# Kernel optimization log

Hardware: AMD Instinct MI355X
Metric: run time of the kernel (lower is better)

## Reference

```python
import jax, jax.numpy as jnp
import numpy as np

NUM_STEPS = 8
THRESHOLD = 0.5


def _glorot(key, shape):
    fan_in = shape[0]
    return jax.random.normal(key, shape, dtype=jnp.float32) / np.sqrt(fan_in).astype(np.float32)


def setup_inputs() -> dict:
    key = jax.random.key(0)
    ks = jax.random.split(key, 24)
    B, APM = 2048, 32           # molecules, atoms per molecule
    N = B * APM                 # 65536 nodes
    E = N * 4                   # 262144 directed edges
    NF, EF, NH, EH, MA = 64, 16, 128, 128, 256
    inp = {}
    inp['mol_a_reprs'] = jax.random.normal(ks[0], (B, MA), dtype=jnp.float32)
    inp['node_features'] = jax.random.normal(ks[1], (N, NF), dtype=jnp.float32)
    inp['edge_features'] = jax.random.normal(ks[2], (E, EF), dtype=jnp.float32)
    inp['node_hidden0'] = jnp.zeros((N, NH), dtype=jnp.float32)
    inp['edge_hidden0'] = jnp.zeros((E, EH), dtype=jnp.float32)
    inp['edges'] = jax.random.randint(ks[3], (2, E), 0, N, dtype=jnp.int32)
    inp['batch_indices'] = jnp.repeat(jnp.arange(B, dtype=jnp.int32), APM)  # sorted, in-range
    # MPN weights (no bias)
    inp['W1'] = _glorot(ks[4], (NF, EH))   # src node features -> edge hidden
    inp['W2'] = _glorot(ks[5], (EF, EH))   # edge features -> edge hidden
    inp['W3'] = _glorot(ks[6], (NH, EH))   # src node hidden -> edge hidden
    inp['U1'] = _glorot(ks[7], (NF, NH))   # node features -> node hidden
    inp['U2'] = _glorot(ks[8], (EH, NH))   # aggregated edge hidden -> node hidden
    # pick-atom MLP: (MA+NH)->256->128->64->1
    inp['M1w'] = _glorot(ks[9], (MA + NH, 256)); inp['M1b'] = jnp.zeros((256,), jnp.float32)
    inp['M2w'] = _glorot(ks[10], (256, 128));    inp['M2b'] = jnp.zeros((128,), jnp.float32)
    inp['M3w'] = _glorot(ks[11], (128, 64));     inp['M3b'] = jnp.zeros((64,), jnp.float32)
    inp['M4w'] = _glorot(ks[12], (64, 1));       inp['M4b'] = jnp.zeros((1,), jnp.float32)
    return inp


def _mpn(node_features, edge_features, node_h, edge_h, src, dst, W1, W2, W3, U1, U2):
    N = node_features.shape[0]
    W1x_src = node_features[src] @ W1          # [E, EH], loop-invariant
    W2e = edge_features @ W2                   # [E, EH], loop-invariant
    U1x = node_features @ U1                   # [N, NH], loop-invariant
    for _ in range(NUM_STEPS):
        agg = jax.ops.segment_sum(edge_h, dst, num_segments=N)   # [N, EH]
        node_h = jax.nn.relu(U1x + agg @ U2)                     # [N, NH]
        edge_h = jax.nn.relu(W1x_src + W2e + node_h[src] @ W3)   # [E, EH]
    return node_h


def reference(mol_a_reprs, node_features, edge_features, node_hidden0, edge_hidden0,
              edges, batch_indices, W1, W2, W3, U1, U2,
              M1w, M1b, M2w, M2b, M3w, M3b, M4w, M4b):
    src, dst = edges[0], edges[1]
    node_h = _mpn(node_features, edge_features, node_hidden0, edge_hidden0,
                  src, dst, W1, W2, W3, U1, U2)
    b_atom_mol_a = mol_a_reprs[batch_indices]                    # index_select gather [N, MA]
    x = jnp.concatenate([node_h, b_atom_mol_a], axis=1)          # [N, NH+MA]
    x = jax.nn.relu(x @ M1w + M1b)
    x = jax.nn.relu(x @ M2w + M2b)
    x = jax.nn.relu(x @ M3w + M3b)
    p = jax.nn.sigmoid(x @ M4w + M4b)                            # [N, 1]
    return p >= THRESHOLD
```

## Files before the change

kernel.cpp:

```cpp
#include <hip/hip_runtime.h>
#include <cstddef>

#define NF 64
#define EF 16
#define NH 128
#define EH 128
#define MA 256

static inline int ceil_div(int a, int b) { return (a + b - 1) / b; }

__global__ __launch_bounds__(256) void gemm128_kernel(
    const float* __restrict__ A, const float* __restrict__ Bw,
    float* __restrict__ C,
    const float* __restrict__ addR, const int* __restrict__ addIdx,
    const float* __restrict__ bias, const int* __restrict__ gatherA,
    int M, int K, int Nc, int doRelu, int reluA)
{
    __shared__ float As[16][132];
    __shared__ float Bs[16][132];
    const int tid = threadIdx.x;
    const int tx = tid & 15;
    const int ty = tid >> 4;
    const int m0 = blockIdx.y << 7;
    const int n0 = blockIdx.x << 7;

    const int lr = tid >> 1;
    const int lc = (tid & 1) << 3;
    const int br = tid >> 4;
    const int bc = (tid & 15) << 3;

    float acc[8][8];
#pragma unroll
    for (int i = 0; i < 8; ++i)
#pragma unroll
        for (int j = 0; j < 8; ++j) acc[i][j] = 0.0f;

    int arow = gatherA ? gatherA[m0 + lr] : (m0 + lr);
    const float* aptr = A + (size_t)arow * K + lc;

    for (int k0 = 0; k0 < K; k0 += 16) {
        float4 a0 = *(const float4*)(aptr + k0);
        float4 a1 = *(const float4*)(aptr + k0 + 4);
        float4 b0 = *(const float4*)(Bw + (size_t)(k0 + br) * Nc + n0 + bc);
        float4 b1 = *(const float4*)(Bw + (size_t)(k0 + br) * Nc + n0 + bc + 4);
        if (reluA) {
            a0.x = fmaxf(a0.x, 0.f); a0.y = fmaxf(a0.y, 0.f); a0.z = fmaxf(a0.z, 0.f); a0.w = fmaxf(a0.w, 0.f);
            a1.x = fmaxf(a1.x, 0.f); a1.y = fmaxf(a1.y, 0.f); a1.z = fmaxf(a1.z, 0.f); a1.w = fmaxf(a1.w, 0.f);
        }
        __syncthreads();
        As[lc + 0][lr] = a0.x; As[lc + 1][lr] = a0.y; As[lc + 2][lr] = a0.z; As[lc + 3][lr] = a0.w;
        As[lc + 4][lr] = a1.x; As[lc + 5][lr] = a1.y; As[lc + 6][lr] = a1.z; As[lc + 7][lr] = a1.w;
        *(float4*)&Bs[br][bc] = b0;
        *(float4*)&Bs[br][bc + 4] = b1;
        __syncthreads();
#pragma unroll
        for (int kk = 0; kk < 16; ++kk) {
            float4 av0 = *(const float4*)&As[kk][ty * 8];
            float4 av1 = *(const float4*)&As[kk][ty * 8 + 4];
            float4 bv0 = *(const float4*)&Bs[kk][tx * 8];
            float4 bv1 = *(const float4*)&Bs[kk][tx * 8 + 4];
            float a[8] = {av0.x, av0.y, av0.z, av0.w, av1.x, av1.y, av1.z, av1.w};
            float b[8] = {bv0.x, bv0.y, bv0.z, bv0.w, bv1.x, bv1.y, bv1.z, bv1.w};
#pragma unroll
            for (int i = 0; i < 8; ++i)
#pragma unroll
                for (int j = 0; j < 8; ++j)
                    acc[i][j] = fmaf(a[i], b[j], acc[i][j]);
        }
    }

    const int c = n0 + tx * 8;
    float4 bvl = make_float4(0.f, 0.f, 0.f, 0.f), bvh = bvl;
    if (bias) { bvl = *(const float4*)(bias + c); bvh = *(const float4*)(bias + c + 4); }
#pragma unroll
    for (int i = 0; i < 8; ++i) {
        int r = m0 + ty * 8 + i;
        float4 vl = make_float4(acc[i][0], acc[i][1], acc[i][2], acc[i][3]);
        float4 vh = make_float4(acc[i][4], acc[i][5], acc[i][6], acc[i][7]);
        if (addR) {
            int ar = addIdx ? addIdx[r] : r;
            float4 al = *(const float4*)(addR + (size_t)ar * Nc + c);
            float4 ah = *(const float4*)(addR + (size_t)ar * Nc + c + 4);
            vl.x += al.x; vl.y += al.y; vl.z += al.z; vl.w += al.w;
            vh.x += ah.x; vh.y += ah.y; vh.z += ah.z; vh.w += ah.w;
        }
        vl.x += bvl.x; vl.y += bvl.y; vl.z += bvl.z; vl.w += bvl.w;
        vh.x += bvh.x; vh.y += bvh.y; vh.z += bvh.z; vh.w += bvh.w;
        if (doRelu) {
            vl.x = fmaxf(vl.x, 0.f); vl.y = fmaxf(vl.y, 0.f); vl.z = fmaxf(vl.z, 0.f); vl.w = fmaxf(vl.w, 0.f);
            vh.x = fmaxf(vh.x, 0.f); vh.y = fmaxf(vh.y, 0.f); vh.z = fmaxf(vh.z, 0.f); vh.w = fmaxf(vh.w, 0.f);
        }
        *(float4*)(C + (size_t)r * Nc + c) = vl;
        *(float4*)(C + (size_t)r * Nc + c + 4) = vh;
    }
}

__global__ __launch_bounds__(256, 2) void fused_step_kernel(
    const float* __restrict__ nodeT_in, const float* __restrict__ W2eS,
    const int* __restrict__ rp, const int* __restrict__ srcS,
    const float* __restrict__ U1x, const float* __restrict__ U2,
    const float* __restrict__ nodePre, const float* __restrict__ W3,
    float* __restrict__ nodeT_out, float* __restrict__ node_h_out,
    int writeNodeH, int doGemm2)
{
    __shared__ float As[128][132];
    __shared__ float Bs[16][132];
    const int tid = threadIdx.x;
    const int m0 = blockIdx.x << 7;

    {
        const int cx = (tid & 31) << 2;
        const int ry = tid >> 5;
        for (int rg = 0; rg < 16; ++rg) {
            const int row = rg * 8 + ry;
            const int n = m0 + row;
            const int p0 = rp[n], p1 = rp[n + 1];
            float4 s = make_float4(0.f, 0.f, 0.f, 0.f);
            for (int p = p0; p < p1; ++p) {
                const int sn = srcS[p];
                float4 t = *(const float4*)(nodeT_in + (size_t)sn * EH + cx);
                float4 w = *(const float4*)(W2eS + (size_t)p * EH + cx);
                s.x += fmaxf(t.x + w.x, 0.f);
                s.y += fmaxf(t.y + w.y, 0.f);
                s.z += fmaxf(t.z + w.z, 0.f);
                s.w += fmaxf(t.w + w.w, 0.f);
            }
            As[cx + 0][row] = s.x;
            As[cx + 1][row] = s.y;
            As[cx + 2][row] = s.z;
            As[cx + 3][row] = s.w;
        }
    }
    __syncthreads();

    const int tx = tid & 15, ty = tid >> 4;
    const int br = tid >> 4, bc = (tid & 15) << 3;

    float acc[8][8];
#pragma unroll
    for (int i = 0; i < 8; ++i)
#pragma unroll
        for (int j = 0; j < 8; ++j) acc[i][j] = 0.0f;

#define FUSED_GEMM(WPTR)                                                          \
    for (int k0 = 0; k0 < 128; k0 += 16) {                                        \
        float4 b0 = *(const float4*)(WPTR + (size_t)(k0 + br) * 128 + bc);        \
        float4 b1 = *(const float4*)(WPTR + (size_t)(k0 + br) * 128 + bc + 4);    \
        __syncthreads();                                                          \
        *(float4*)&Bs[br][bc] = b0;                                               \
        *(float4*)&Bs[br][bc + 4] = b1;                                           \
        __syncthreads();                                                          \
        _Pragma("unroll")                                                         \
        for (int kk = 0; kk < 16; ++kk) {                                         \
            float4 av0 = *(const float4*)&As[k0 + kk][ty * 8];                    \
            float4 av1 = *(const float4*)&As[k0 + kk][ty * 8 + 4];                \
            float4 bv0 = *(const float4*)&Bs[kk][tx * 8];                         \
            float4 bv1 = *(const float4*)&Bs[kk][tx * 8 + 4];                     \
            float a[8] = {av0.x, av0.y, av0.z, av0.w, av1.x, av1.y, av1.z, av1.w};\
            float b[8] = {bv0.x, bv0.y, bv0.z, bv0.w, bv1.x, bv1.y, bv1.z, bv1.w};\
            _Pragma("unroll")                                                     \
            for (int i = 0; i < 8; ++i)                                           \
                _Pragma("unroll")                                                 \
                for (int j = 0; j < 8; ++j)                                       \
                    acc[i][j] = fmaf(a[i], b[j], acc[i][j]);                      \
        }                                                                         \
    }

    FUSED_GEMM(U2)

    const int c = tx * 8;
#pragma unroll
    for (int i = 0; i < 8; ++i) {
        const int r = m0 + ty * 8 + i;
        float4 u0 = *(const float4*)(U1x + (size_t)r * NH + c);
        float4 u1 = *(const float4*)(U1x + (size_t)r * NH + c + 4);
        acc[i][0] = fmaxf(acc[i][0] + u0.x, 0.f);
        acc[i][1] = fmaxf(acc[i][1] + u0.y, 0.f);
        acc[i][2] = fmaxf(acc[i][2] + u0.z, 0.f);
        acc[i][3] = fmaxf(acc[i][3] + u0.w, 0.f);
        acc[i][4] = fmaxf(acc[i][4] + u1.x, 0.f);
        acc[i][5] = fmaxf(acc[i][5] + u1.y, 0.f);
        acc[i][6] = fmaxf(acc[i][6] + u1.z, 0.f);
        acc[i][7] = fmaxf(acc[i][7] + u1.w, 0.f);
    }
    if (writeNodeH) {
#pragma unroll
        for (int i = 0; i < 8; ++i) {
            const int r = m0 + ty * 8 + i;
            *(float4*)(node_h_out + (size_t)r * NH + c) =
                make_float4(acc[i][0], acc[i][1], acc[i][2], acc[i][3]);
            *(float4*)(node_h_out + (size_t)r * NH + c + 4) =
                make_float4(acc[i][4], acc[i][5], acc[i][6], acc[i][7]);
        }
    }
    if (!doGemm2) return;

    __syncthreads();
#pragma unroll
    for (int i = 0; i < 8; ++i)
#pragma unroll
        for (int j = 0; j < 8; ++j)
            As[tx * 8 + j][ty * 8 + i] = acc[i][j];
    __syncthreads();

#pragma unroll
    for (int i = 0; i < 8; ++i)
#pragma unroll
        for (int j = 0; j < 8; ++j) acc[i][j] = 0.0f;

    FUSED_GEMM(W3)
#undef FUSED_GEMM

#pragma unroll
    for (int i = 0; i < 8; ++i) {
        const int r = m0 + ty * 8 + i;
        float4 p0 = *(const float4*)(nodePre + (size_t)r * EH + c);
        float4 p1 = *(const float4*)(nodePre + (size_t)r * EH + c + 4);
        *(float4*)(nodeT_out + (size_t)r * EH + c) =
            make_float4(acc[i][0] + p0.x, acc[i][1] + p0.y, acc[i][2] + p0.z, acc[i][3] + p0.w);
        *(float4*)(nodeT_out + (size_t)r * EH + c + 4) =
            make_float4(acc[i][4] + p1.x, acc[i][5] + p1.y, acc[i][6] + p1.z, acc[i][7] + p1.w);
    }
}

__global__ __launch_bounds__(256) void hist_kernel(const int* __restrict__ dst, int* __restrict__ deg, int E) {
    int e = blockIdx.x * 256 + threadIdx.x;
    if (e < E) atomicAdd(&deg[dst[e]], 1);
}

__global__ __launch_bounds__(256) void scan_block_kernel(const int* __restrict__ deg, int* __restrict__ rp,
                                                         int* __restrict__ bsum) {
    __shared__ int buf[256];
    int tid = threadIdx.x;
    int i = blockIdx.x * 256 + tid;
    int v = deg[i];
    buf[tid] = v;
    __syncthreads();
    for (int off = 1; off < 256; off <<= 1) {
        int t = (tid >= off) ? buf[tid - off] : 0;
        __syncthreads();
        buf[tid] += t;
        __syncthreads();
    }
    rp[i] = buf[tid] - v;
    if (tid == 255) bsum[blockIdx.x] = buf[255];
}

__global__ __launch_bounds__(256) void scan_top_kernel(const int* __restrict__ bsum, int* __restrict__ boff,
                                                       int* __restrict__ rp, int N) {
    __shared__ int buf[256];
    int tid = threadIdx.x;
    int v = bsum[tid];
    buf[tid] = v;
    __syncthreads();
    for (int off = 1; off < 256; off <<= 1) {
        int t = (tid >= off) ? buf[tid - off] : 0;
        __syncthreads();
        buf[tid] += t;
        __syncthreads();
    }
    boff[tid] = buf[tid] - v;
    if (tid == 255) rp[N] = buf[255];
}

__global__ __launch_bounds__(256) void scan_add_kernel(int* __restrict__ rp, int* __restrict__ cursor,
                                                       const int* __restrict__ boff) {
    int tid = threadIdx.x;
    int i = blockIdx.x * 256 + tid;
    int v = rp[i] + boff[blockIdx.x];
    rp[i] = v;
    cursor[i] = v;
}

__global__ __launch_bounds__(256) void scatter_kernel(const int* __restrict__ dst, const int* __restrict__ src,
                                                      int* __restrict__ cursor,
                                                      int* __restrict__ eid, int* __restrict__ srcS, int E) {
    int e = blockIdx.x * 256 + threadIdx.x;
    if (e < E) {
        int p = atomicAdd(&cursor[dst[e]], 1);
        eid[p] = e;
        srcS[p] = src[e];
    }
}

__global__ __launch_bounds__(256) void x3final_kernel(const float* __restrict__ x2, const float* __restrict__ M3w,
                                                      const float* __restrict__ b3, const float* __restrict__ M4w,
                                                      const float* __restrict__ b4, int* __restrict__ out) {
    __shared__ float As[16][132];
    __shared__ float Bs[16][68];
    __shared__ float red[128][17];
    const int tid = threadIdx.x;
    const int tx = tid & 15;
    const int ty = tid >> 4;
    const int m0 = blockIdx.x << 7;
    const int lr = tid >> 1, lc = (tid & 1) << 3;
    const int br = tid >> 4, bc = (tid & 15) << 2;

    float acc[8][4];
#pragma unroll
    for (int i = 0; i < 8; ++i)
#pragma unroll
        for (int j = 0; j < 4; ++j) acc[i][j] = 0.0f;

    const float* aptr = x2 + (size_t)(m0 + lr) * 128 + lc;
    for (int k0 = 0; k0 < 128; k0 += 16) {
        float4 a0 = *(const float4*)(aptr + k0);
        float4 a1 = *(const float4*)(aptr + k0 + 4);
        float4 bv = *(const float4*)(M3w + (size_t)(k0 + br) * 64 + bc);
        __syncthreads();
        As[lc + 0][lr] = a0.x; As[lc + 1][lr] = a0.y; As[lc + 2][lr] = a0.z; As[lc + 3][lr] = a0.w;
        As[lc + 4][lr] = a1.x; As[lc + 5][lr] = a1.y; As[lc + 6][lr] = a1.z; As[lc + 7][lr] = a1.w;
        *(float4*)&Bs[br][bc] = bv;
        __syncthreads();
#pragma unroll
        for (int kk = 0; kk < 16; ++kk) {
            float4 av0 = *(const float4*)&As[kk][ty * 8];
            float4 av1 = *(const float4*)&As[kk][ty * 8 + 4];
            float4 bv0 = *(const float4*)&Bs[kk][tx * 4];
            float a[8] = {av0.x, av0.y, av0.z, av0.w, av1.x, av1.y, av1.z, av1.w};
            float b[4] = {bv0.x, bv0.y, bv0.z, bv0.w};
#pragma unroll
            for (int i = 0; i < 8; ++i)
#pragma unroll
                for (int j = 0; j < 4; ++j)
                    acc[i][j] = fmaf(a[i], b[j], acc[i][j]);
        }
    }

    const int c = tx * 4;
    float4 b3v = *(const float4*)(b3 + c);
    float4 w4v = *(const float4*)(M4w + c);
#pragma unroll
    for (int i = 0; i < 8; ++i) {
        float p = fmaxf(acc[i][0] + b3v.x, 0.f) * w4v.x
                + fmaxf(acc[i][1] + b3v.y, 0.f) * w4v.y
                + fmaxf(acc[i][2] + b3v.z, 0.f) * w4v.z
                + fmaxf(acc[i][3] + b3v.w, 0.f) * w4v.w;
        red[ty * 8 + i][tx] = p;
    }
    __syncthreads();
    if (tid < 128) {
        float z = b4[0];
#pragma unroll
        for (int j = 0; j < 16; ++j) z += red[tid][j];
        out[m0 + tid] = z >= 0.f ? 1 : 0;
    }
}

extern "C" void kernel_launch(void* const* d_in, const int* in_sizes, int n_in,
                              void* d_out, int out_size, void* d_ws, size_t ws_size,
                              hipStream_t stream)
{
    const float* mol_a = (const float*)d_in[0];
    const float* nf    = (const float*)d_in[1];
    const float* ef    = (const float*)d_in[2];
    const int*   edges = (const int*)d_in[5];
    const int*   batch = (const int*)d_in[6];
    const float* W1  = (const float*)d_in[7];
    const float* W2  = (const float*)d_in[8];
    const float* W3  = (const float*)d_in[9];
    const float* U1  = (const float*)d_in[10];
    const float* U2  = (const float*)d_in[11];
    const float* M1w = (const float*)d_in[12];
    const float* M1b = (const float*)d_in[13];
    const float* M2w = (const float*)d_in[14];
    const float* M2b = (const float*)d_in[15];
    const float* M3w = (const float*)d_in[16];
    const float* M3b = (const float*)d_in[17];
    const float* M4w = (const float*)d_in[18];
    const float* M4b = (const float*)d_in[19];

    const int N = in_sizes[3] / NH;
    const int E = in_sizes[4] / EH;
    const int B = in_sizes[0] / MA;
    const int* srcp = edges;
    const int* dstp = edges + E;

    char* ws = (char*)d_ws;
    size_t off = 0;
    auto alloc = [&](size_t bytes) -> char* {
        char* p = ws + off;
        off = (off + bytes + 255) & ~(size_t)255;
        return p;
    };
    int* deg     = (int*)alloc((size_t)N * 4);
    int* rp      = (int*)alloc(((size_t)N + 1) * 4);
    int* cursor  = (int*)alloc((size_t)N * 4);
    int* bsum    = (int*)alloc(256 * 4);
    int* boff    = (int*)alloc(256 * 4);
    int* eid     = (int*)alloc((size_t)E * 4);
    int* srcS    = (int*)alloc((size_t)E * 4);
    float* nodePre = (float*)alloc((size_t)N * EH * 4);
    float* U1x     = (float*)alloc((size_t)N * NH * 4);
    float* node_h  = (float*)alloc((size_t)N * NH * 4);
    float* nodeTa  = (float*)alloc((size_t)N * EH * 4);
    float* nodeTb  = (float*)alloc((size_t)N * EH * 4);
    float* molPart = (float*)alloc((size_t)B * 256 * 4);
    float* W2eS    = (float*)alloc((size_t)E * EH * 4);
    float* x1 = (float*)W2eS;
    float* x2 = nodeTa;

    hipMemsetAsync(deg, 0, (size_t)N * 4, stream);
    hist_kernel<<<ceil_div(E, 256), 256, 0, stream>>>(dstp, deg, E);
    scan_block_kernel<<<N / 256, 256, 0, stream>>>(deg, rp, bsum);
    scan_top_kernel<<<1, 256, 0, stream>>>(bsum, boff, rp, N);
    scan_add_kernel<<<N / 256, 256, 0, stream>>>(rp, cursor, boff);
    scatter_kernel<<<ceil_div(E, 256), 256, 0, stream>>>(dstp, srcp, cursor, eid, srcS, E);

    gemm128_kernel<<<dim3(1, N / 128), 256, 0, stream>>>(nf, W1, nodePre, nullptr, nullptr, nullptr, nullptr, N, NF, EH, 0, 0);
    gemm128_kernel<<<dim3(1, E / 128), 256, 0, stream>>>(ef, W2, W2eS, nullptr, nullptr, nullptr, eid, E, EF, EH, 0, 0);
    gemm128_kernel<<<dim3(1, N / 128), 256, 0, stream>>>(nf, U1, U1x, nullptr, nullptr, nullptr, nullptr, N, NF, NH, 0, 0);

    gemm128_kernel<<<dim3(1, N / 128), 256, 0, stream>>>(U1x, W3, nodeTa, nodePre, nullptr, nullptr, nullptr, N, NH, EH, 0, 1);

    float* curT = nodeTa;
    float* nxtT = nodeTb;
    for (int s = 0; s < 6; ++s) {
        fused_step_kernel<<<N / 128, 256, 0, stream>>>(curT, W2eS, rp, srcS, U1x, U2, nodePre, W3,
                                                       nxtT, nullptr, 0, 1);
        float* t = curT; curT = nxtT; nxtT = t;
    }
    fused_step_kernel<<<N / 128, 256, 0, stream>>>(curT, W2eS, rp, srcS, U1x, U2, nodePre, W3,
                                                   nxtT, node_h, 1, 0);

    gemm128_kernel<<<dim3(2, B / 128), 256, 0, stream>>>(mol_a, M1w + 128 * 256, molPart, nullptr, nullptr, M1b, nullptr, B, MA, 256, 0, 0);
    gemm128_kernel<<<dim3(2, N / 128), 256, 0, stream>>>(node_h, M1w, x1, molPart, batch, nullptr, nullptr, N, NH, 256, 1, 0);
    gemm128_kernel<<<dim3(1, N / 128), 256, 0, stream>>>(x1, M2w, x2, nullptr, nullptr, M2b, nullptr, N, 256, 128, 1, 0);
    x3final_kernel<<<N / 128, 256, 0, stream>>>(x2, M3w, M3b, M4w, M4b, (int*)d_out);
}
```

Baseline: 1.448 ms.

## Recompute edge-feature projection on the fly and split fused step into agg+GEMMs

Drops the precomputed E×128 W2e buffer. Edge features are permuted once into dst-sorted order (16 floats per edge), and each aggregation pass recomputes ef·W2 with W2 held in registers. This cuts per-step traffic from streaming 128 MB of W2eS to 16 MB plus extra FMAs. The fused per-step kernel is also split into an aggregation kernel and two separate 64-row-tile GEMMs. That adds intermediate round-trips through global memory for agg and node_h but gives smaller tiles and more blocks.

```diff
diff --git a/kernel.cpp b/kernel.cpp
--- a/kernel.cpp
+++ b/kernel.cpp
@@ -9,60 +9,57 @@
 
 static inline int ceil_div(int a, int b) { return (a + b - 1) / b; }
 
-__global__ __launch_bounds__(256) void gemm128_kernel(
+__global__ __launch_bounds__(256) void gemm64_kernel(
     const float* __restrict__ A, const float* __restrict__ Bw,
     float* __restrict__ C,
     const float* __restrict__ addR, const int* __restrict__ addIdx,
-    const float* __restrict__ bias, const int* __restrict__ gatherA,
+    const float* __restrict__ bias,
     int M, int K, int Nc, int doRelu, int reluA)
 {
-    __shared__ float As[16][132];
+    __shared__ float As[16][68];
     __shared__ float Bs[16][132];
     const int tid = threadIdx.x;
     const int tx = tid & 15;
     const int ty = tid >> 4;
-    const int m0 = blockIdx.y << 7;
+    const int m0 = blockIdx.y << 6;
     const int n0 = blockIdx.x << 7;
 
-    const int lr = tid >> 1;
-    const int lc = (tid & 1) << 3;
+    const int lr = tid >> 2;
+    const int lc = (tid & 3) << 2;
     const int br = tid >> 4;
     const int bc = (tid & 15) << 3;
 
-    float acc[8][8];
-#pragma unroll
-    for (int i = 0; i < 8; ++i)
+    float acc[4][8];
+#pragma unroll
+    for (int i = 0; i < 4; ++i)
 #pragma unroll
         for (int j = 0; j < 8; ++j) acc[i][j] = 0.0f;
 
-    int arow = gatherA ? gatherA[m0 + lr] : (m0 + lr);
-    const float* aptr = A + (size_t)arow * K + lc;
+    const float* aptr = A + (size_t)(m0 + lr) * K + lc;
 
     for (int k0 = 0; k0 < K; k0 += 16) {
-        float4 a0 = *(const float4*)(aptr + k0);
-        float4 a1 = *(const float4*)(aptr + k0 + 4);
+        float4 a4 = *(const float4*)(aptr + k0);
         float4 b0 = *(const float4*)(Bw + (size_t)(k0 + br) * Nc + n0 + bc);
         float4 b1 = *(const float4*)(Bw + (size_t)(k0 + br) * Nc + n0 + bc + 4);
         if (reluA) {
-            a0.x = fmaxf(a0.x, 0.f); a0.y = fmaxf(a0.y, 0.f); a0.z = fmaxf(a0.z, 0.f); a0.w = fmaxf(a0.w, 0.f);
-            a1.x = fmaxf(a1.x, 0.f); a1.y = fmaxf(a1.y, 0.f); a1.z = fmaxf(a1.z, 0.f); a1.w = fmaxf(a1.w, 0.f);
-        }
-        __syncthreads();
-        As[lc + 0][lr] = a0.x; As[lc + 1][lr] = a0.y; As[lc + 2][lr] = a0.z; As[lc + 3][lr] = a0.w;
-        As[lc + 4][lr] = a1.x; As[lc + 5][lr] = a1.y; As[lc + 6][lr] = a1.z; As[lc + 7][lr] = a1.w;
+            a4.x = fmaxf(a4.x, 0.f); a4.y = fmaxf(a4.y, 0.f);
+            a4.z = fmaxf(a4.z, 0.f); a4.w = fmaxf(a4.w, 0.f);
+        }
+        __syncthreads();
+        As[lc + 0][lr] = a4.x; As[lc + 1][lr] = a4.y;
+        As[lc + 2][lr] = a4.z; As[lc + 3][lr] = a4.w;
         *(float4*)&Bs[br][bc] = b0;
         *(float4*)&Bs[br][bc + 4] = b1;
         __syncthreads();
 #pragma unroll
         for (int kk = 0; kk < 16; ++kk) {
-            float4 av0 = *(const float4*)&As[kk][ty * 8];
-            float4 av1 = *(const float4*)&As[kk][ty * 8 + 4];
+            float4 av = *(const float4*)&As[kk][ty * 4];
             float4 bv0 = *(const float4*)&Bs[kk][tx * 8];
             float4 bv1 = *(const float4*)&Bs[kk][tx * 8 + 4];
-            float a[8] = {av0.x, av0.y, av0.z, av0.w, av1.x, av1.y, av1.z, av1.w};
+            float a[4] = {av.x, av.y, av.z, av.w};
             float b[8] = {bv0.x, bv0.y, bv0.z, bv0.w, bv1.x, bv1.y, bv1.z, bv1.w};
 #pragma unroll
-            for (int i = 0; i < 8; ++i)
+            for (int i = 0; i < 4; ++i)
 #pragma unroll
                 for (int j = 0; j < 8; ++j)
                     acc[i][j] = fmaf(a[i], b[j], acc[i][j]);
@@ -73,8 +70,8 @@
     float4 bvl = make_float4(0.f, 0.f, 0.f, 0.f), bvh = bvl;
     if (bias) { bvl = *(const float4*)(bias + c); bvh = *(const float4*)(bias + c + 4); }
 #pragma unroll
-    for (int i = 0; i < 8; ++i) {
-        int r = m0 + ty * 8 + i;
+    for (int i = 0; i < 4; ++i) {
+        int r = m0 + ty * 4 + i;
         float4 vl = make_float4(acc[i][0], acc[i][1], acc[i][2], acc[i][3]);
         float4 vh = make_float4(acc[i][4], acc[i][5], acc[i][6], acc[i][7]);
         if (addR) {
@@ -92,134 +89,6 @@
         }
         *(float4*)(C + (size_t)r * Nc + c) = vl;
         *(float4*)(C + (size_t)r * Nc + c + 4) = vh;
-    }
-}
-
-__global__ __launch_bounds__(256, 2) void fused_step_kernel(
-    const float* __restrict__ nodeT_in, const float* __restrict__ W2eS,
-    const int* __restrict__ rp, const int* __restrict__ srcS,
-    const float* __restrict__ U1x, const float* __restrict__ U2,
-    const float* __restrict__ nodePre, const float* __restrict__ W3,
-    float* __restrict__ nodeT_out, float* __restrict__ node_h_out,
-    int writeNodeH, int doGemm2)
-{
-    __shared__ float As[128][132];
-    __shared__ float Bs[16][132];
-    const int tid = threadIdx.x;
-    const int m0 = blockIdx.x << 7;
-
-    {
-        const int cx = (tid & 31) << 2;
-        const int ry = tid >> 5;
-        for (int rg = 0; rg < 16; ++rg) {
-            const int row = rg * 8 + ry;
-            const int n = m0 + row;
-            const int p0 = rp[n], p1 = rp[n + 1];
-            float4 s = make_float4(0.f, 0.f, 0.f, 0.f);
-            for (int p = p0; p < p1; ++p) {
-                const int sn = srcS[p];
-                float4 t = *(const float4*)(nodeT_in + (size_t)sn * EH + cx);
-                float4 w = *(const float4*)(W2eS + (size_t)p * EH + cx);
-                s.x += fmaxf(t.x + w.x, 0.f);
-                s.y += fmaxf(t.y + w.y, 0.f);
-                s.z += fmaxf(t.z + w.z, 0.f);
-                s.w += fmaxf(t.w + w.w, 0.f);
-            }
-            As[cx + 0][row] = s.x;
-            As[cx + 1][row] = s.y;
-            As[cx + 2][row] = s.z;
-            As[cx + 3][row] = s.w;
-        }
-    }
-    __syncthreads();
-
-    const int tx = tid & 15, ty = tid >> 4;
-    const int br = tid >> 4, bc = (tid & 15) << 3;
-
-    float acc[8][8];
-#pragma unroll
-    for (int i = 0; i < 8; ++i)
-#pragma unroll
-        for (int j = 0; j < 8; ++j) acc[i][j] = 0.0f;
-
-#define FUSED_GEMM(WPTR)                                                          \
-    for (int k0 = 0; k0 < 128; k0 += 16) {                                        \
-        float4 b0 = *(const float4*)(WPTR + (size_t)(k0 + br) * 128 + bc);        \
-        float4 b1 = *(const float4*)(WPTR + (size_t)(k0 + br) * 128 + bc + 4);    \
-        __syncthreads();                                                          \
-        *(float4*)&Bs[br][bc] = b0;                                               \
-        *(float4*)&Bs[br][bc + 4] = b1;                                           \
-        __syncthreads();                                                          \
-        _Pragma("unroll")                                                         \
-        for (int kk = 0; kk < 16; ++kk) {                                         \
-            float4 av0 = *(const float4*)&As[k0 + kk][ty * 8];                    \
-            float4 av1 = *(const float4*)&As[k0 + kk][ty * 8 + 4];                \
-            float4 bv0 = *(const float4*)&Bs[kk][tx * 8];                         \
-            float4 bv1 = *(const float4*)&Bs[kk][tx * 8 + 4];                     \
-            float a[8] = {av0.x, av0.y, av0.z, av0.w, av1.x, av1.y, av1.z, av1.w};\
-            float b[8] = {bv0.x, bv0.y, bv0.z, bv0.w, bv1.x, bv1.y, bv1.z, bv1.w};\
-            _Pragma("unroll")                                                     \
-            for (int i = 0; i < 8; ++i)                                           \
-                _Pragma("unroll")                                                 \
-                for (int j = 0; j < 8; ++j)                                       \
-                    acc[i][j] = fmaf(a[i], b[j], acc[i][j]);                      \
-        }                                                                         \
-    }
-
-    FUSED_GEMM(U2)
-
-    const int c = tx * 8;
-#pragma unroll
-    for (int i = 0; i < 8; ++i) {
-        const int r = m0 + ty * 8 + i;
-        float4 u0 = *(const float4*)(U1x + (size_t)r * NH + c);
-        float4 u1 = *(const float4*)(U1x + (size_t)r * NH + c + 4);
-        acc[i][0] = fmaxf(acc[i][0] + u0.x, 0.f);
-        acc[i][1] = fmaxf(acc[i][1] + u0.y, 0.f);
-        acc[i][2] = fmaxf(acc[i][2] + u0.z, 0.f);
-        acc[i][3] = fmaxf(acc[i][3] + u0.w, 0.f);
-        acc[i][4] = fmaxf(acc[i][4] + u1.x, 0.f);
-        acc[i][5] = fmaxf(acc[i][5] + u1.y, 0.f);
-        acc[i][6] = fmaxf(acc[i][6] + u1.z, 0.f);
-        acc[i][7] = fmaxf(acc[i][7] + u1.w, 0.f);
-    }
-    if (writeNodeH) {
-#pragma unroll
-        for (int i = 0; i < 8; ++i) {
-            const int r = m0 + ty * 8 + i;
-            *(float4*)(node_h_out + (size_t)r * NH + c) =
-                make_float4(acc[i][0], acc[i][1], acc[i][2], acc[i][3]);
-            *(float4*)(node_h_out + (size_t)r * NH + c + 4) =
-                make_float4(acc[i][4], acc[i][5], acc[i][6], acc[i][7]);
-        }
-    }
-    if (!doGemm2) return;
-
-    __syncthreads();
-#pragma unroll
-    for (int i = 0; i < 8; ++i)
-#pragma unroll
-        for (int j = 0; j < 8; ++j)
-            As[tx * 8 + j][ty * 8 + i] = acc[i][j];
-    __syncthreads();
-
-#pragma unroll
-    for (int i = 0; i < 8; ++i)
-#pragma unroll
-        for (int j = 0; j < 8; ++j) acc[i][j] = 0.0f;
-
-    FUSED_GEMM(W3)
-#undef FUSED_GEMM
-
-#pragma unroll
-    for (int i = 0; i < 8; ++i) {
-        const int r = m0 + ty * 8 + i;
-        float4 p0 = *(const float4*)(nodePre + (size_t)r * EH + c);
-        float4 p1 = *(const float4*)(nodePre + (size_t)r * EH + c + 4);
-        *(float4*)(nodeT_out + (size_t)r * EH + c) =
-            make_float4(acc[i][0] + p0.x, acc[i][1] + p0.y, acc[i][2] + p0.z, acc[i][3] + p0.w);
-        *(float4*)(nodeT_out + (size_t)r * EH + c + 4) =
-            make_float4(acc[i][4] + p1.x, acc[i][5] + p1.y, acc[i][6] + p1.z, acc[i][7] + p1.w);
     }
 }
 
@@ -281,6 +150,54 @@
         eid[p] = e;
         srcS[p] = src[e];
     }
+}
+
+__global__ __launch_bounds__(256) void gather_ef_kernel(const float* __restrict__ ef, const int* __restrict__ eid,
+                                                        float* __restrict__ efS, int E) {
+    int idx = blockIdx.x * 256 + threadIdx.x;
+    int p = idx >> 2, comp = idx & 3;
+    if (p < E) {
+        int e = eid[p];
+        float4 v = *(const float4*)(ef + (size_t)e * EF + comp * 4);
+        *(float4*)(efS + (size_t)p * EF + comp * 4) = v;
+    }
+}
+
+__global__ __launch_bounds__(256) void agg_kernel(const float* __restrict__ nodeT, const float* __restrict__ efS,
+                                                  const int* __restrict__ rp, const int* __restrict__ srcS,
+                                                  const float* __restrict__ W2, float* __restrict__ agg) {
+    const int n = blockIdx.x * 8 + threadIdx.y;
+    const int c = threadIdx.x << 2;
+    float4 w2r[16];
+#pragma unroll
+    for (int k = 0; k < 16; ++k) w2r[k] = *(const float4*)(W2 + (size_t)k * EH + c);
+
+    const int p0 = rp[n], p1 = rp[n + 1];
+    float4 s = make_float4(0.f, 0.f, 0.f, 0.f);
+    for (int p = p0; p < p1; ++p) {
+        const int sn = srcS[p];
+        const float* ep = efS + (size_t)p * EF;
+        float4 e0 = *(const float4*)(ep);
+        float4 e1 = *(const float4*)(ep + 4);
+        float4 e2 = *(const float4*)(ep + 8);
+        float4 e3 = *(const float4*)(ep + 12);
+        float ef16[16] = {e0.x, e0.y, e0.z, e0.w, e1.x, e1.y, e1.z, e1.w,
+                          e2.x, e2.y, e2.z, e2.w, e3.x, e3.y, e3.z, e3.w};
+        float4 w = make_float4(0.f, 0.f, 0.f, 0.f);
+#pragma unroll
+        for (int k = 0; k < 16; ++k) {
+            w.x = fmaf(ef16[k], w2r[k].x, w.x);
+            w.y = fmaf(ef16[k], w2r[k].y, w.y);
+            w.z = fmaf(ef16[k], w2r[k].z, w.z);
+            w.w = fmaf(ef16[k], w2r[k].w, w.w);
+        }
+        float4 t = *(const float4*)(nodeT + (size_t)sn * EH + c);
+        s.x += fmaxf(t.x + w.x, 0.f);
+        s.y += fmaxf(t.y + w.y, 0.f);
+        s.z += fmaxf(t.z + w.z, 0.f);
+        s.w += fmaxf(t.w + w.w, 0.f);
+    }
+    *(float4*)(agg + (size_t)n * EH + c) = s;
 }
 
 __global__ __launch_bounds__(256) void x3final_kernel(const float* __restrict__ x2, const float* __restrict__ M3w,
@@ -390,14 +307,15 @@
     int* boff    = (int*)alloc(256 * 4);
     int* eid     = (int*)alloc((size_t)E * 4);
     int* srcS    = (int*)alloc((size_t)E * 4);
+    float* efS     = (float*)alloc((size_t)E * EF * 4);
     float* nodePre = (float*)alloc((size_t)N * EH * 4);
     float* U1x     = (float*)alloc((size_t)N * NH * 4);
     float* node_h  = (float*)alloc((size_t)N * NH * 4);
     float* nodeTa  = (float*)alloc((size_t)N * EH * 4);
     float* nodeTb  = (float*)alloc((size_t)N * EH * 4);
+    float* aggp    = (float*)alloc((size_t)N * EH * 4);
     float* molPart = (float*)alloc((size_t)B * 256 * 4);
-    float* W2eS    = (float*)alloc((size_t)E * EH * 4);
-    float* x1 = (float*)W2eS;
+    float* x1      = (float*)alloc((size_t)N * 256 * 4);
     float* x2 = nodeTa;
 
     hipMemsetAsync(deg, 0, (size_t)N * 4, stream);
@@ -406,25 +324,26 @@
     scan_top_kernel<<<1, 256, 0, stream>>>(bsum, boff, rp, N);
     scan_add_kernel<<<N / 256, 256, 0, stream>>>(rp, cursor, boff);
     scatter_kernel<<<ceil_div(E, 256), 256, 0, stream>>>(dstp, srcp, cursor, eid, srcS, E);
-
-    gemm128_kernel<<<dim3(1, N / 128), 256, 0, stream>>>(nf, W1, nodePre, nullptr, nullptr, nullptr, nullptr, N, NF, EH, 0, 0);
-    gemm128_kernel<<<dim3(1, E / 128), 256, 0, stream>>>(ef, W2, W2eS, nullptr, nullptr, nullptr, eid, E, EF, EH, 0, 0);
-    gemm128_kernel<<<dim3(1, N / 128), 256, 0, stream>>>(nf, U1, U1x, nullptr, nullptr, nullptr, nullptr, N, NF, NH, 0, 0);
-
-    gemm128_kernel<<<dim3(1, N / 128), 256, 0, stream>>>(U1x, W3, nodeTa, nodePre, nullptr, nullptr, nullptr, N, NH, EH, 0, 1);
+    gather_ef_kernel<<<ceil_div(E * 4, 256), 256, 0, stream>>>(ef, eid, efS, E);
+
+    gemm64_kernel<<<dim3(1, N / 64), 256, 0, stream>>>(nf, W1, nodePre, nullptr, nullptr, nullptr, N, NF, EH, 0, 0);
+    gemm64_kernel<<<dim3(1, N / 64), 256, 0, stream>>>(nf, U1, U1x, nullptr, nullptr, nullptr, N, NF, NH, 0, 0);
+
+    gemm64_kernel<<<dim3(1, N / 64), 256, 0, stream>>>(U1x, W3, nodeTa, nodePre, nullptr, nullptr, N, NH, EH, 0, 1);
 
     float* curT = nodeTa;
     float* nxtT = nodeTb;
     for (int s = 0; s < 6; ++s) {
-        fused_step_kernel<<<N / 128, 256, 0, stream>>>(curT, W2eS, rp, srcS, U1x, U2, nodePre, W3,
-                                                       nxtT, nullptr, 0, 1);
+        agg_kernel<<<N / 8, dim3(32, 8), 0, stream>>>(curT, efS, rp, srcS, W2, aggp);
+        gemm64_kernel<<<dim3(1, N / 64), 256, 0, stream>>>(aggp, U2, node_h, U1x, nullptr, nullptr, N, EH, NH, 1, 0);
+        gemm64_kernel<<<dim3(1, N / 64), 256, 0, stream>>>(node_h, W3, nxtT, nodePre, nullptr, nullptr, N, NH, EH, 0, 0);
         float* t = curT; curT = nxtT; nxtT = t;
     }
-    fused_step_kernel<<<N / 128, 256, 0, stream>>>(curT, W2eS, rp, srcS, U1x, U2, nodePre, W3,
-                                                   nxtT, node_h, 1, 0);
-
-    gemm128_kernel<<<dim3(2, B / 128), 256, 0, stream>>>(mol_a, M1w + 128 * 256, molPart, nullptr, nullptr, M1b, nullptr, B, MA, 256, 0, 0);
-    gemm128_kernel<<<dim3(2, N / 128), 256, 0, stream>>>(node_h, M1w, x1, molPart, batch, nullptr, nullptr, N, NH, 256, 1, 0);
-    gemm128_kernel<<<dim3(1, N / 128), 256, 0, stream>>>(x1, M2w, x2, nullptr, nullptr, M2b, nullptr, N, 256, 128, 1, 0);
+    agg_kernel<<<N / 8, dim3(32, 8), 0, stream>>>(curT, efS, rp, srcS, W2, aggp);
+    gemm64_kernel<<<dim3(1, N / 64), 256, 0, stream>>>(aggp, U2, node_h, U1x, nullptr, nullptr, N, EH, NH, 1, 0);
+
+    gemm64_kernel<<<dim3(2, B / 64), 256, 0, stream>>>(mol_a, M1w + 128 * 256, molPart, nullptr, nullptr, M1b, B, MA, 256, 0, 0);
+    gemm64_kernel<<<dim3(2, N / 64), 256, 0, stream>>>(node_h, M1w, x1, molPart, batch, nullptr, N, NH, 256, 1, 0);
+    gemm64_kernel<<<dim3(1, N / 64), 256, 0, stream>>>(x1, M2w, x2, nullptr, nullptr, M2b, N, 256, 128, 1, 0);
     x3final_kernel<<<N / 128, 256, 0, stream>>>(x2, M3w, M3b, M4w, M4b, (int*)d_out);
 }
```

Measured after the change: 1.258 ms. -13.1%, faster.
